# Optimization experiments

Measured on AMD Instinct MI355X. Metric: run time of the kernel, lower is better.

## Reference

```python
import jax, jax.numpy as jnp
import numpy as np

TYPE_NUM = 40000
REL_NUM = 10000
N = TYPE_NUM + REL_NUM  # 50000 nodes
E = 800000              # edges (avg degree 16)
EMB, MID, OUT = 256, 256, 128


def setup_inputs() -> dict:
    key = jax.random.key(0)
    k0, k1, k2, k3 = jax.random.split(key, 4)
    # xavier-ish scales
    node_emb = jax.random.normal(k0, (N, EMB), jnp.float32) * (1.0 / np.sqrt(EMB))
    W1 = jax.random.normal(k1, (EMB, MID), jnp.float32) * (1.0 / np.sqrt(EMB))
    W2 = jax.random.normal(k2, (MID, OUT), jnp.float32) * (1.0 / np.sqrt(MID))
    b1 = jnp.zeros((MID,), jnp.float32)
    b2 = jnp.zeros((OUT,), jnp.float32)
    edge_index = jax.random.randint(k3, (2, E), 0, N, jnp.int32)
    return {"node_emb": node_emb, "W1": W1, "b1": b1, "W2": W2, "b2": b2,
            "edge_index": edge_index}


def _gcn_conv(X, W, b, src, dst):
    """torch_geometric GCNConv: x' = D^-1/2 (A+I) D^-1/2 (X W) + b."""
    n = X.shape[0]
    loop = jnp.arange(n, dtype=src.dtype)
    s = jnp.concatenate([src, loop])  # source j
    d = jnp.concatenate([dst, loop])  # target i
    deg = jax.ops.segment_sum(jnp.ones_like(d, dtype=X.dtype), d, num_segments=n)
    dis = jnp.where(deg > 0, jax.lax.rsqrt(deg), 0.0)
    h = X @ W                               # [n, out]
    norm = (dis[s] * dis[d])[:, None]       # [E+n, 1]
    msg = h[s] * norm                       # gather messages
    return jax.ops.segment_sum(msg, d, num_segments=n) + b


def reference(node_emb, W1, b1, W2, b2, edge_index):
    src, dst = edge_index[0], edge_index[1]
    # torch nn.GELU default is exact (erf) gelu
    X = jax.nn.gelu(_gcn_conv(node_emb, W1, b1, src, dst), approximate=False)
    X = jax.nn.gelu(_gcn_conv(X, W2, b2, src, dst), approximate=False)
    return X[:TYPE_NUM], X[TYPE_NUM:]
```

## Files before the change

### kernel.cpp

```cpp
#include <hip/hip_runtime.h>
#include <math.h>

#define EMB 256
#define MID 256
#define OUTF 128
#define KDIM 256
#define LDK 40
#define SLOT 64
#define NBIN 64

using frag_ab = __attribute__((ext_vector_type(8))) short;
using frag_cd = __attribute__((ext_vector_type(4))) float;
typedef float f32x2 __attribute__((ext_vector_type(2)));
typedef float f32x4 __attribute__((ext_vector_type(4)));
typedef unsigned int u32x2 __attribute__((ext_vector_type(2)));
typedef unsigned int u32x4 __attribute__((ext_vector_type(4)));

__device__ __forceinline__ float gelu_exact(float x) {
    return 0.5f * x * (1.0f + erff(x * 0.70710678118654752f));
}

__device__ __forceinline__ unsigned short f2bf(float f) {
    union { float f; unsigned int i; } v;
    v.f = f;
    unsigned int r = v.i + 0x7fff + ((v.i >> 16) & 1);
    return (unsigned short)(r >> 16);
}

__device__ __forceinline__ f32x2 bfpair(unsigned int u) {
    union { unsigned int i; float f; } a, b;
    a.i = u << 16;
    b.i = u & 0xffff0000u;
    f32x2 r;
    r.x = a.f; r.y = b.f;
    return r;
}


__global__ __launch_bounds__(256) void init_kernel(
    const float* __restrict__ W1, const float* __restrict__ W2,
    unsigned short* __restrict__ W1t, unsigned short* __restrict__ W2t,
    int* __restrict__ cnt, unsigned short* __restrict__ h1,
    unsigned short* __restrict__ h2, int* __restrict__ ghist, int n, int zb) {
    int b = blockIdx.x;
    int tid = threadIdx.x;
    if (b < zb) {
        int i = b * 256 + tid;
        if (i < n) cnt[i] = 0;
        return;
    }
    b -= zb;
    if (b < 256) {
        int id = b * 256 + tid;
        int k = id >> 8, nn = id & 255;
        W1t[(size_t)nn * EMB + k] = f2bf(W1[(size_t)k * MID + nn]);
        return;
    }
    b -= 256;
    if (b < 128) {
        int id = b * 256 + tid;
        int k = id >> 7, nn = id & 127;
        W2t[(size_t)nn * MID + k] = f2bf(W2[(size_t)k * OUTF + nn]);
        return;
    }
    size_t Np1 = (size_t)n + 1;
    int s = tid >> 5, c = tid & 31;
    h1[((size_t)s * Np1 + n) * 32 + c] = 0;
    if (tid < 128) h2[((size_t)s * Np1 + n) * 32 + c] = 0;
    if (tid < NBIN) ghist[tid] = 0;
}


__global__ void rank_scatter(const int* __restrict__ src, const int* __restrict__ dst,
                             int* __restrict__ cnt, unsigned short* __restrict__ slots,
                             int E) {
    int e = blockIdx.x * blockDim.x + threadIdx.x;
    if (e < E) {
        int d = dst[e];
        int r = atomicAdd(&cnt[d], 1);
        if (r < SLOT) slots[(size_t)d * SLOT + r] = (unsigned short)src[e];
    }
}


__global__ __launch_bounds__(256) void deg_hist(const int* __restrict__ cnt,
                                                int* __restrict__ ghist, int n) {
    __shared__ int lh[NBIN];
    int tid = threadIdx.x;
    if (tid < NBIN) lh[tid] = 0;
    __syncthreads();
    int i = blockIdx.x * 256 + tid;
    if (i < n) {
        int d = cnt[i];
        d = d < NBIN - 1 ? d : NBIN - 1;
        atomicAdd(&lh[d], 1);
    }
    __syncthreads();
    if (tid < NBIN && lh[tid]) atomicAdd(&ghist[tid], lh[tid]);
}

__global__ void deg_scan(const int* __restrict__ ghist, int* __restrict__ goff) {
    int v = ghist[threadIdx.x];
    int x = v;
#pragma unroll
    for (int d = 1; d < NBIN; d <<= 1) {
        int t = __shfl_up(x, d);
        if ((int)threadIdx.x >= d) x += t;
    }
    goff[threadIdx.x] = x - v;
}

__global__ __launch_bounds__(256) void deg_scatter(const int* __restrict__ cnt,
                                                   int* __restrict__ goff,
                                                   int* __restrict__ perm, int n) {
    __shared__ int lh[NBIN], lbase[NBIN];
    int tid = threadIdx.x;
    if (tid < NBIN) lh[tid] = 0;
    __syncthreads();
    int i = blockIdx.x * 256 + tid;
    int d = 0, rl = 0;
    if (i < n) {
        d = cnt[i];
        d = d < NBIN - 1 ? d : NBIN - 1;
        rl = atomicAdd(&lh[d], 1);
    }
    __syncthreads();
    if (tid < NBIN) lbase[tid] = lh[tid] ? atomicAdd(&goff[tid], lh[tid]) : 0;
    __syncthreads();
    if (i < n) perm[lbase[d] + rl] = i;
}


template <bool A_FP32, int NT>
__global__ __launch_bounds__(256, 2) void mfma_gemm(const void* __restrict__ Av,
                                                    const unsigned short* __restrict__ Wt,
                                                    const int* __restrict__ cnt,
                                                    unsigned short* __restrict__ C,
                                                    int M, int Cs) {
    __shared__ __align__(16) unsigned short As[128 * LDK];
    __shared__ __align__(16) unsigned short Bs[NT * 128 * LDK];

    const int tid = threadIdx.x;
    const int m0 = blockIdx.x * 128;
    const int wave = tid >> 6, lane = tid & 63;
    const int wrow = (wave >> 1) * 64, wcol = (wave & 1) * 64;
    const int q = lane >> 4, r = lane & 15;

    frag_cd acc[NT][4][4] = {};

    const int qb = tid & 3;
    const int nb = tid >> 2;

    for (int ks = 0; ks < KDIM; ks += 32) {
        if (A_FP32) {
            const float* A = (const float*)Av;
            int qa = tid & 7;
            int ra = tid >> 3;
#pragma unroll
            for (int rr = 0; rr < 4; ++rr) {
                int row = ra + rr * 32;
                int grow = m0 + row;
                if (grow >= M) grow = M - 1;
                float4 v = *(const float4*)(A + (size_t)grow * KDIM + ks + qa * 4);
                ushort4 w;
                w.x = f2bf(v.x); w.y = f2bf(v.y); w.z = f2bf(v.z); w.w = f2bf(v.w);
                *(ushort4*)&As[row * LDK + qa * 4] = w;
            }
        } else {
            const unsigned short* A = (const unsigned short*)Av;
#pragma unroll
            for (int rr = 0; rr < 2; ++rr) {
                int row = nb + rr * 64;
                int grow = m0 + row;
                if (grow >= M) grow = M - 1;
                uint4 v = *(const uint4*)(A + ((size_t)(ks >> 5) * M + grow) * 32 + qb * 8);
                *(uint4*)&As[row * LDK + qb * 8] = v;
            }
        }
#pragma unroll
        for (int rr = 0; rr < 2 * NT; ++rr) {
            int n = nb + rr * 64;
            uint4 v = *(const uint4*)(Wt + (size_t)n * KDIM + ks + qb * 8);
            *(uint4*)&Bs[n * LDK + qb * 8] = v;
        }
        __syncthreads();

        frag_ab af[4];
#pragma unroll
        for (int i = 0; i < 4; ++i)
            af[i] = *(const frag_ab*)&As[(wrow + i * 16 + r) * LDK + q * 8];
#pragma unroll
        for (int nt = 0; nt < NT; ++nt) {
            frag_ab bfr[4];
#pragma unroll
            for (int j = 0; j < 4; ++j)
                bfr[j] = *(const frag_ab*)&Bs[(nt * 128 + wcol + j * 16 + r) * LDK + q * 8];
#pragma unroll
            for (int i = 0; i < 4; ++i)
#pragma unroll
                for (int j = 0; j < 4; ++j)
                    acc[nt][i][j] = __builtin_amdgcn_mfma_f32_16x16x32_bf16(
                        af[i], bfr[j], acc[nt][i][j], 0, 0, 0);
        }
        __syncthreads();
    }

#pragma unroll
    for (int i = 0; i < 4; ++i)
#pragma unroll
        for (int g = 0; g < 4; ++g) {
            int row = m0 + wrow + i * 16 + q * 4 + g;
            if (row < M) {
                float sc = rsqrtf((float)(cnt[row] + 1));
#pragma unroll
                for (int nt = 0; nt < NT; ++nt)
#pragma unroll
                    for (int j = 0; j < 4; ++j) {
                        int col = nt * 128 + wcol + j * 16 + r;
                        C[((size_t)(col >> 5) * Cs + row) * 32 + (col & 31)] =
                            f2bf(acc[nt][i][j][g] * sc);
                    }
            }
        }
}


template <int NS, bool OUT_BF>
__global__ __launch_bounds__(256, 4) void agg_slice(
    const unsigned short* __restrict__ H,
    const int* __restrict__ cnt,
    const unsigned short* __restrict__ slots,
    const int* __restrict__ perm,
    const float* __restrict__ bias,
    void* __restrict__ out,
    int n) {
    constexpr int XPS = 8 / NS;
    const int bid = blockIdx.x;
    const int xg = bid & 7;
    const int s = xg / XPS;
    const int w = (bid >> 3) * XPS + (xg % XPS);
    const int W = (int)(gridDim.x >> 3) * XPS;
    const int wave = threadIdx.x >> 6, lane = threadIdx.x & 63;
    const int g = lane >> 2, r = lane & 3;
    const size_t Np1 = (size_t)n + 1;
    const unsigned short* Hs = H + (size_t)s * Np1 * 32;
    const int r8 = r * 8;
    const f32x4 bv0 = *(const f32x4*)(bias + s * 32 + r8);
    const f32x4 bv1 = *(const f32x4*)(bias + s * 32 + r8 + 4);

    for (int nd0 = (w * 4 + wave) * 16; nd0 < n; nd0 += W * 64) {
        int idx = nd0 + g;
        bool valid = idx < n;
        int ndg = perm[valid ? idx : n - 1];
        int deg = cnt[ndg];
        float di = rsqrtf((float)(deg + 1));
        int m = valid ? (deg < SLOT ? deg : SLOT) : 0;
        int mm = m;
        mm = max(mm, __shfl_xor(mm, 4));
        mm = max(mm, __shfl_xor(mm, 8));
        mm = max(mm, __shfl_xor(mm, 16));
        mm = max(mm, __shfl_xor(mm, 32));

        u32x4 sv = *(const u32x4*)(Hs + (size_t)ndg * 32 + r8);
        f32x2 a0 = bfpair(sv.x), a1 = bfpair(sv.y), a2 = bfpair(sv.z), a3 = bfpair(sv.w);

        const unsigned short* sl = slots + (size_t)ndg * SLOT;
        u32x4 sq0 = {}, sq1 = {};
        if (r8 < m) sq0 = __builtin_nontemporal_load((const u32x4*)(sl + r8));
        if (32 + r8 < m) sq1 = __builtin_nontemporal_load((const u32x4*)(sl + 32 + r8));

        if (mm > 0) {
            u32x4 A[4], B[4];
            auto load4 = [&](u32x4* buf, int t) {
                int srcl = (lane & 60) | ((t >> 3) & 3);
                u32x4 sq = (t < 32) ? sq0 : sq1;
                unsigned hw0, hw1;
                if (t & 4) { hw0 = sq.z; hw1 = sq.w; } else { hw0 = sq.x; hw1 = sq.y; }
                unsigned w0 = (unsigned)__shfl((int)hw0, srcl);
                unsigned w1 = (unsigned)__shfl((int)hw1, srcl);
                int j0 = (t + 0 < m) ? (int)(w0 & 0xffffu) : n;
                int j1 = (t + 1 < m) ? (int)(w0 >> 16) : n;
                int j2 = (t + 2 < m) ? (int)(w1 & 0xffffu) : n;
                int j3 = (t + 3 < m) ? (int)(w1 >> 16) : n;
                buf[0] = *(const u32x4*)(Hs + (size_t)j0 * 32 + r8);
                buf[1] = *(const u32x4*)(Hs + (size_t)j1 * 32 + r8);
                buf[2] = *(const u32x4*)(Hs + (size_t)j2 * 32 + r8);
                buf[3] = *(const u32x4*)(Hs + (size_t)j3 * 32 + r8);
            };
            auto acc4 = [&](const u32x4* buf) {
#pragma unroll
                for (int u = 0; u < 4; ++u) {
                    a0 += bfpair(buf[u].x);
                    a1 += bfpair(buf[u].y);
                    a2 += bfpair(buf[u].z);
                    a3 += bfpair(buf[u].w);
                }
            };

            load4(A, 0);
            int t = 4;
            for (;;) {
                if (t >= mm) { acc4(A); break; }
                load4(B, t); acc4(A); t += 4;
                if (t >= mm) { acc4(B); break; }
                load4(A, t); acc4(B); t += 4;
            }
        }

        float res[8];
        res[0] = gelu_exact(di * a0.x + bv0.x);
        res[1] = gelu_exact(di * a0.y + bv0.y);
        res[2] = gelu_exact(di * a1.x + bv0.z);
        res[3] = gelu_exact(di * a1.y + bv0.w);
        res[4] = gelu_exact(di * a2.x + bv1.x);
        res[5] = gelu_exact(di * a2.y + bv1.y);
        res[6] = gelu_exact(di * a3.x + bv1.z);
        res[7] = gelu_exact(di * a3.y + bv1.w);

        if (valid) {
            if (OUT_BF) {
                u32x4 pk;
                pk.x = (unsigned int)f2bf(res[0]) | ((unsigned int)f2bf(res[1]) << 16);
                pk.y = (unsigned int)f2bf(res[2]) | ((unsigned int)f2bf(res[3]) << 16);
                pk.z = (unsigned int)f2bf(res[4]) | ((unsigned int)f2bf(res[5]) << 16);
                pk.w = (unsigned int)f2bf(res[6]) | ((unsigned int)f2bf(res[7]) << 16);
                unsigned short* ob = (unsigned short*)out + ((size_t)s * n + ndg) * 32 + r8;
                __builtin_nontemporal_store(pk, (u32x4*)ob);
            } else {
                f32x4 rv0, rv1;
                rv0.x = res[0]; rv0.y = res[1]; rv0.z = res[2]; rv0.w = res[3];
                rv1.x = res[4]; rv1.y = res[5]; rv1.z = res[6]; rv1.w = res[7];
                float* ob = (float*)out + (size_t)ndg * (NS * 32) + s * 32 + r8;
                __builtin_nontemporal_store(rv0, (f32x4*)ob);
                __builtin_nontemporal_store(rv1, (f32x4*)(ob + 4));
            }
        }
    }
}


extern "C" void kernel_launch(void* const* d_in, const int* in_sizes, int n_in,
                              void* d_out, int out_size, void* d_ws, size_t ws_size,
                              hipStream_t stream) {
    const float* node_emb = (const float*)d_in[0];
    const float* W1 = (const float*)d_in[1];
    const float* b1 = (const float*)d_in[2];
    const float* W2 = (const float*)d_in[3];
    const float* b2 = (const float*)d_in[4];
    const int* edge_index = (const int*)d_in[5];

    const int N = in_sizes[0] / EMB;
    const int E = in_sizes[5] / 2;
    const int* src = edge_index;
    const int* dst = edge_index + E;

    char* ws = (char*)d_ws;
    size_t off = 0;
    auto alloc = [&](size_t bytes) -> void* {
        off = (off + 255) & ~(size_t)255;
        void* p = ws + off;
        off += bytes;
        return p;
    };

    const int nb = (N + 255) / 256;

    int* cnt = (int*)alloc((size_t)N * 4);
    unsigned short* slots = (unsigned short*)alloc((size_t)N * SLOT * 2);
    unsigned short* W1t = (unsigned short*)alloc((size_t)EMB * MID * 2);
    unsigned short* W2t = (unsigned short*)alloc((size_t)MID * OUTF * 2);
    unsigned short* h1 = (unsigned short*)alloc((size_t)(N + 1) * MID * 2);
    unsigned short* h2 = (unsigned short*)alloc((size_t)(N + 1) * OUTF * 2);
    unsigned short* X1 = (unsigned short*)alloc((size_t)N * MID * 2);
    int* ghist = (int*)alloc(NBIN * 4);
    int* goff = (int*)alloc(NBIN * 4);
    int* perm = (int*)alloc((size_t)N * 4);

    init_kernel<<<nb + 256 + 128 + 1, 256, 0, stream>>>(
        W1, W2, W1t, W2t, cnt, h1, h2, ghist, N, nb);
    rank_scatter<<<(E + 255) / 256, 256, 0, stream>>>(src, dst, cnt, slots, E);
    deg_hist<<<nb, 256, 0, stream>>>(cnt, ghist, N);
    deg_scan<<<1, NBIN, 0, stream>>>(ghist, goff);
    deg_scatter<<<nb, 256, 0, stream>>>(cnt, goff, perm, N);
    mfma_gemm<true, 2><<<(N + 127) / 128, 256, 0, stream>>>(node_emb, W1t, cnt, h1, N, N + 1);
    agg_slice<8, true><<<2048, 256, 0, stream>>>(h1, cnt, slots, perm, b1, X1, N);
    mfma_gemm<false, 1><<<(N + 127) / 128, 256, 0, stream>>>(X1, W2t, cnt, h2, N, N + 1);
    agg_slice<4, false><<<2048, 256, 0, stream>>>(h2, cnt, slots, perm, b2, d_out, N);
}
```

Before: 272.4 us.

## Prefill neighbor slots with dummy index and prefetch next node in aggregation

The slot table is pre-filled with the padding row index n in init_kernel, so the aggregation loop can drop its per-neighbor bounds selects and load the first slot chunk unconditionally. The aggregation loop is also software-pipelined: perm, degree, self row and first slot chunk for the next node group are loaded during the current group's reduction, hiding that dependent-load latency. The cost is an extra 6.4MB memset of the slots buffer every call, plus more live registers that may reduce occupancy.

```diff
diff --git a/kernel.cpp b/kernel.cpp
--- a/kernel.cpp
+++ b/kernel.cpp
@@ -41,7 +41,8 @@
     const float* __restrict__ W1, const float* __restrict__ W2,
     unsigned short* __restrict__ W1t, unsigned short* __restrict__ W2t,
     int* __restrict__ cnt, unsigned short* __restrict__ h1,
-    unsigned short* __restrict__ h2, int* __restrict__ ghist, int n, int zb) {
+    unsigned short* __restrict__ h2, int* __restrict__ ghist,
+    unsigned short* __restrict__ slots, int sfb, int n, int zb) {
     int b = blockIdx.x;
     int tid = threadIdx.x;
     if (b < zb) {
@@ -61,6 +62,16 @@
         int id = b * 256 + tid;
         int k = id >> 7, nn = id & 127;
         W2t[(size_t)nn * MID + k] = f2bf(W2[(size_t)k * OUTF + nn]);
+        return;
+    }
+    b -= 128;
+    if (b < sfb) {
+        int i = b * 256 + tid;
+        if (i < n * (SLOT / 4)) {
+            unsigned pat = (unsigned)n | ((unsigned)n << 16);
+            u32x2 v; v.x = pat; v.y = pat;
+            ((u32x2*)slots)[i] = v;
+        }
         return;
     }
     size_t Np1 = (size_t)n + 1;
@@ -247,56 +258,69 @@
     const int r8 = r * 8;
     const f32x4 bv0 = *(const f32x4*)(bias + s * 32 + r8);
     const f32x4 bv1 = *(const f32x4*)(bias + s * 32 + r8 + 4);
-
-    for (int nd0 = (w * 4 + wave) * 16; nd0 < n; nd0 += W * 64) {
-        int idx = nd0 + g;
-        bool valid = idx < n;
-        int ndg = perm[valid ? idx : n - 1];
-        int deg = cnt[ndg];
+    const int stride = W * 64;
+
+    int nd0 = (w * 4 + wave) * 16;
+    if (nd0 >= n) return;
+
+    int idx0 = nd0 + g;
+    int ndg = perm[idx0 < n ? idx0 : n - 1];
+    int deg = cnt[ndg];
+    u32x4 sv = *(const u32x4*)(Hs + (size_t)ndg * 32 + r8);
+    u32x4 sq0 = __builtin_nontemporal_load((const u32x4*)(slots + (size_t)ndg * SLOT + r8));
+    u32x4 sq1 = {};
+
+    for (;;) {
+        const int nnd0 = nd0 + stride;
+        const bool more = nnd0 < n;
+        int pndg = 0;
+        if (more) {
+            int nidx = nnd0 + g;
+            pndg = perm[nidx < n ? nidx : n - 1];
+        }
+
         float di = rsqrtf((float)(deg + 1));
-        int m = valid ? (deg < SLOT ? deg : SLOT) : 0;
+        int m = deg < SLOT ? deg : SLOT;
         int mm = m;
         mm = max(mm, __shfl_xor(mm, 4));
         mm = max(mm, __shfl_xor(mm, 8));
         mm = max(mm, __shfl_xor(mm, 16));
         mm = max(mm, __shfl_xor(mm, 32));
 
-        u32x4 sv = *(const u32x4*)(Hs + (size_t)ndg * 32 + r8);
         f32x2 a0 = bfpair(sv.x), a1 = bfpair(sv.y), a2 = bfpair(sv.z), a3 = bfpair(sv.w);
 
-        const unsigned short* sl = slots + (size_t)ndg * SLOT;
-        u32x4 sq0 = {}, sq1 = {};
-        if (r8 < m) sq0 = __builtin_nontemporal_load((const u32x4*)(sl + r8));
-        if (32 + r8 < m) sq1 = __builtin_nontemporal_load((const u32x4*)(sl + 32 + r8));
+        if (mm > 32)
+            sq1 = __builtin_nontemporal_load(
+                (const u32x4*)(slots + (size_t)ndg * SLOT + 32 + r8));
+
+        u32x4 A[4], B[4];
+        auto load4 = [&](u32x4* buf, int t) {
+            int srcl = (lane & 60) | ((t >> 3) & 3);
+            u32x4 sq = (t < 32) ? sq0 : sq1;
+            unsigned hw0, hw1;
+            if (t & 4) { hw0 = sq.z; hw1 = sq.w; } else { hw0 = sq.x; hw1 = sq.y; }
+            unsigned w0 = (unsigned)__shfl((int)hw0, srcl);
+            unsigned w1 = (unsigned)__shfl((int)hw1, srcl);
+            int j0 = (int)(w0 & 0xffffu);
+            int j1 = (int)(w0 >> 16);
+            int j2 = (int)(w1 & 0xffffu);
+            int j3 = (int)(w1 >> 16);
+            buf[0] = *(const u32x4*)(Hs + (size_t)j0 * 32 + r8);
+            buf[1] = *(const u32x4*)(Hs + (size_t)j1 * 32 + r8);
+            buf[2] = *(const u32x4*)(Hs + (size_t)j2 * 32 + r8);
+            buf[3] = *(const u32x4*)(Hs + (size_t)j3 * 32 + r8);
+        };
+        auto acc4 = [&](const u32x4* buf) {
+#pragma unroll
+            for (int u = 0; u < 4; ++u) {
+                a0 += bfpair(buf[u].x);
+                a1 += bfpair(buf[u].y);
+                a2 += bfpair(buf[u].z);
+                a3 += bfpair(buf[u].w);
+            }
+        };
 
         if (mm > 0) {
-            u32x4 A[4], B[4];
-            auto load4 = [&](u32x4* buf, int t) {
-                int srcl = (lane & 60) | ((t >> 3) & 3);
-                u32x4 sq = (t < 32) ? sq0 : sq1;
-                unsigned hw0, hw1;
-                if (t & 4) { hw0 = sq.z; hw1 = sq.w; } else { hw0 = sq.x; hw1 = sq.y; }
-                unsigned w0 = (unsigned)__shfl((int)hw0, srcl);
-                unsigned w1 = (unsigned)__shfl((int)hw1, srcl);
-                int j0 = (t + 0 < m) ? (int)(w0 & 0xffffu) : n;
-                int j1 = (t + 1 < m) ? (int)(w0 >> 16) : n;
-                int j2 = (t + 2 < m) ? (int)(w1 & 0xffffu) : n;
-                int j3 = (t + 3 < m) ? (int)(w1 >> 16) : n;
-                buf[0] = *(const u32x4*)(Hs + (size_t)j0 * 32 + r8);
-                buf[1] = *(const u32x4*)(Hs + (size_t)j1 * 32 + r8);
-                buf[2] = *(const u32x4*)(Hs + (size_t)j2 * 32 + r8);
-                buf[3] = *(const u32x4*)(Hs + (size_t)j3 * 32 + r8);
-            };
-            auto acc4 = [&](const u32x4* buf) {
-#pragma unroll
-                for (int u = 0; u < 4; ++u) {
-                    a0 += bfpair(buf[u].x);
-                    a1 += bfpair(buf[u].y);
-                    a2 += bfpair(buf[u].z);
-                    a3 += bfpair(buf[u].w);
-                }
-            };
-
             load4(A, 0);
             int t = 4;
             for (;;) {
@@ -305,6 +329,15 @@
                 if (t >= mm) { acc4(B); break; }
                 load4(A, t); acc4(B); t += 4;
             }
+        }
+
+        int pdeg = 0;
+        u32x4 psv = {}, psq0 = {};
+        if (more) {
+            pdeg = cnt[pndg];
+            psv = *(const u32x4*)(Hs + (size_t)pndg * 32 + r8);
+            psq0 = __builtin_nontemporal_load(
+                (const u32x4*)(slots + (size_t)pndg * SLOT + r8));
         }
 
         float res[8];
@@ -317,7 +350,7 @@
         res[6] = gelu_exact(di * a3.x + bv1.z);
         res[7] = gelu_exact(di * a3.y + bv1.w);
 
-        if (valid) {
+        if (nd0 + g < n) {
             if (OUT_BF) {
                 u32x4 pk;
                 pk.x = (unsigned int)f2bf(res[0]) | ((unsigned int)f2bf(res[1]) << 16);
@@ -335,6 +368,13 @@
                 __builtin_nontemporal_store(rv1, (f32x4*)(ob + 4));
             }
         }
+
+        if (!more) break;
+        nd0 = nnd0;
+        ndg = pndg;
+        deg = pdeg;
+        sv = psv;
+        sq0 = psq0;
     }
 }
 
@@ -364,6 +404,7 @@
     };
 
     const int nb = (N + 255) / 256;
+    const int sfb = (N * (SLOT / 4) + 255) / 256;
 
     int* cnt = (int*)alloc((size_t)N * 4);
     unsigned short* slots = (unsigned short*)alloc((size_t)N * SLOT * 2);
@@ -376,8 +417,8 @@
     int* goff = (int*)alloc(NBIN * 4);
     int* perm = (int*)alloc((size_t)N * 4);
 
-    init_kernel<<<nb + 256 + 128 + 1, 256, 0, stream>>>(
-        W1, W2, W1t, W2t, cnt, h1, h2, ghist, N, nb);
+    init_kernel<<<nb + 256 + 128 + sfb + 1, 256, 0, stream>>>(
+        W1, W2, W1t, W2t, cnt, h1, h2, ghist, slots, sfb, N, nb);
     rank_scatter<<<(E + 255) / 256, 256, 0, stream>>>(src, dst, cnt, slots, E);
     deg_hist<<<nb, 256, 0, stream>>>(cnt, ghist, N);
     deg_scan<<<1, NBIN, 0, stream>>>(ghist, goff);
```

Measured after the change: 270.6 us. About the same (-0.7%).
